# Performance work log

Hardware: AMD Instinct MI355X
Metric: run time of the kernel (lower is better)

## Reference

```python
import jax, jax.numpy as jnp
import numpy as np

B, S, I, H, O = 32, 64, 256, 256, 128


def setup_inputs() -> dict:
    key = jax.random.key(0)
    ks = jax.random.split(key, 8)
    init_k = 1.0 / np.sqrt(H)
    F = H + I
    return {
        "sentence": jax.random.normal(ks[0], (B, S, I), dtype=jnp.float32),
        "weight": jax.random.uniform(ks[1], (H, F), minval=-init_k, maxval=init_k, dtype=jnp.float32),
        "weight_lambda": jax.random.uniform(ks[2], (H, F), minval=0.0, maxval=1.0, dtype=jnp.float32),
        "weight_gamma": jax.random.uniform(ks[3], (H, F), minval=-0.001 * init_k, maxval=0.001 * init_k, dtype=jnp.float32),
        "bias": jax.random.uniform(ks[4], (H,), minval=-init_k, maxval=init_k, dtype=jnp.float32),
        "out_w": jax.random.uniform(ks[5], (O, H), minval=-init_k, maxval=init_k, dtype=jnp.float32),
        "out_b": jax.random.uniform(ks[6], (O,), minval=-init_k, maxval=init_k, dtype=jnp.float32),
    }


def reference(sentence, weight, weight_lambda, weight_gamma, bias, out_w, out_b):
    b, s, i = sentence.shape
    h_dim = weight.shape[0]
    f_dim = weight.shape[1]  # h_dim + i
    h0 = jnp.zeros((b, h_dim), dtype=sentence.dtype)
    f0 = jnp.zeros((b, h_dim, f_dim), dtype=sentence.dtype)

    def step(carry, x_t):
        h, f = carry
        total_input = jnp.concatenate([x_t, h], axis=1)          # (b, f_dim)
        total_weights = weight + f                                # (b, h, f_dim)
        pre = jnp.einsum('bf,bhf->bh', total_input, total_weights)
        norm = jnp.sqrt(jnp.sum(total_weights * total_weights, axis=2)) + 1e-16  # (b, h)
        h_new = jnp.tanh(pre / norm + bias)
        f_new = weight_lambda * (f / norm[..., None]) + \
                weight_gamma * jnp.einsum('bh,bf->bhf', h_new, total_input)
        return (h_new, f_new), None

    (h_fin, f_fin), _ = jax.lax.scan(step, (h0, f0), jnp.swapaxes(sentence, 0, 1))
    tag_space = h_fin @ out_w.T + out_b
    return tag_space, h_fin, f_fin
```

## Files before the change

kernel.cpp:

```cpp
#include <hip/hip_runtime.h>

#define Bq 32
#define Sq 64
#define Iq 256
#define Hq 256
#define Oq 128
#define Fq 512
#define WPB 8
#define NT 512

__device__ __forceinline__ float fast_tanh(float v) {
    const float e = __expf(2.0f * v);
    return 1.0f - __fdividef(2.0f, e + 1.0f);
}

__global__ __launch_bounds__(NT, 2) void stpn_main(
    const float* __restrict__ x,
    const float* __restrict__ w,
    const float* __restrict__ wl,
    const float* __restrict__ wgm,
    const float* __restrict__ bias,
    const float* __restrict__ ow,
    const float* __restrict__ ob,
    float* __restrict__ out,
    unsigned long long* __restrict__ hb)
{
    const int blk   = blockIdx.x;
    const int b     = blk & 31;
    const int chunk = blk >> 5;
    const int h0    = chunk * 32;
    const int tid   = threadIdx.x;
    const int lr    = tid & 15;
    const int r     = tid >> 4;
    const int row   = h0 + r;

    __shared__ float ti[2][Fq];

    float fw[32], fl[32], fg[32], ff[32];
    const size_t rowoff = (size_t)row * Fq;
#pragma unroll
    for (int j = 0; j < 8; ++j) {
        const int c = 4 * lr + 64 * j;
        *(float4*)&fw[4*j] = *(const float4*)(w   + rowoff + c);
        *(float4*)&fl[4*j] = *(const float4*)(wl  + rowoff + c);
        *(float4*)&fg[4*j] = *(const float4*)(wgm + rowoff + c);
    }
#pragma unroll
    for (int j = 0; j < 32; ++j) ff[j] = 0.f;

    const float brow = bias[row];
    const float* xb = x + (size_t)b * Sq * Iq;

    float nsq = 0.f;
#pragma unroll
    for (int j = 0; j < 32; ++j) nsq = fmaf(fw[j], fw[j], nsq);
#pragma unroll
    for (int m = 1; m < 16; m <<= 1) nsq += __shfl_xor(nsq, m, 16);
    float inv = __fdividef(1.0f, sqrtf(nsq) + 1e-16f);

    for (int t = 0; t < Sq; ++t) {
        const int p = t & 1;
        if (tid < Iq) {
            ti[p][tid] = xb[(size_t)t * Iq + tid];
        } else {
            const int hh = tid - Iq;
            float hv = 0.f;
            if (t > 0) {
                unsigned long long* slot =
                    hb + (size_t)((t - 1) & 1) * Bq * Hq + (size_t)b * Hq + hh;
                unsigned long long v;
                do {
                    v = __hip_atomic_load(slot, __ATOMIC_RELAXED,
                                          __HIP_MEMORY_SCOPE_AGENT);
                } while ((unsigned)(v >> 32) != (unsigned)t);
                hv = __uint_as_float((unsigned)(v & 0xffffffffu));
            }
            ti[p][Iq + hh] = hv;
        }
        __syncthreads();

        float pre = 0.f;
#pragma unroll
        for (int j = 0; j < 8; ++j) {
            const float4 tv = *(const float4*)&ti[p][4 * lr + 64 * j];
            pre = fmaf(tv.x, fw[4*j+0] + ff[4*j+0], pre);
            pre = fmaf(tv.y, fw[4*j+1] + ff[4*j+1], pre);
            pre = fmaf(tv.z, fw[4*j+2] + ff[4*j+2], pre);
            pre = fmaf(tv.w, fw[4*j+3] + ff[4*j+3], pre);
        }
#pragma unroll
        for (int m = 1; m < 16; m <<= 1) pre += __shfl_xor(pre, m, 16);
        const float hn = fast_tanh(fmaf(pre, inv, brow));

        if (lr == 0) {
            const unsigned long long pk =
                ((unsigned long long)(unsigned)(t + 1) << 32) |
                (unsigned long long)__float_as_uint(hn);
            __hip_atomic_store(
                hb + (size_t)p * Bq * Hq + (size_t)b * Hq + row, pk,
                __ATOMIC_RELAXED, __HIP_MEMORY_SCOPE_AGENT);
        }

#pragma unroll
        for (int j = 0; j < 8; ++j) {
            const float4 tv = *(const float4*)&ti[p][4 * lr + 64 * j];
            ff[4*j+0] = fmaf(fl[4*j+0], ff[4*j+0] * inv, fg[4*j+0] * (hn * tv.x));
            ff[4*j+1] = fmaf(fl[4*j+1], ff[4*j+1] * inv, fg[4*j+1] * (hn * tv.y));
            ff[4*j+2] = fmaf(fl[4*j+2], ff[4*j+2] * inv, fg[4*j+2] * (hn * tv.z));
            ff[4*j+3] = fmaf(fl[4*j+3], ff[4*j+3] * inv, fg[4*j+3] * (hn * tv.w));
        }
        if (t < Sq - 1) {
            nsq = 0.f;
#pragma unroll
            for (int j = 0; j < 32; ++j) {
                const float tw = fw[j] + ff[j];
                nsq = fmaf(tw, tw, nsq);
            }
#pragma unroll
            for (int m = 1; m < 16; m <<= 1) nsq += __shfl_xor(nsq, m, 16);
            inv = __fdividef(1.0f, sqrtf(nsq) + 1e-16f);
        }
    }

    float* fo = out + Bq * Oq + Bq * Hq + (size_t)b * Hq * Fq + rowoff;
#pragma unroll
    for (int j = 0; j < 8; ++j) {
        const int c = 4 * lr + 64 * j;
        *(float4*)(fo + c) = *(const float4*)&ff[4*j];
    }

    if (chunk == 0) {
        if (tid < Hq) {
            unsigned long long* slot =
                hb + (size_t)1 * Bq * Hq + (size_t)b * Hq + tid;
            unsigned long long v;
            do {
                v = __hip_atomic_load(slot, __ATOMIC_RELAXED,
                                      __HIP_MEMORY_SCOPE_AGENT);
            } while ((unsigned)(v >> 32) != (unsigned)Sq);
            const float hv = __uint_as_float((unsigned)(v & 0xffffffffu));
            ti[0][tid] = hv;
            out[Bq * Oq + (size_t)b * Hq + tid] = hv;
        }
        __syncthreads();
        const int o = tid >> 2;
        const int l = tid & 3;
        const float* wr = ow + (size_t)o * Hq + l * 64;
        float acc = 0.f;
#pragma unroll
        for (int k = 0; k < 16; ++k) {
            const float4 w4 = ((const float4*)wr)[k];
            const float4 h4 = *(const float4*)&ti[0][l * 64 + 4 * k];
            acc += w4.x * h4.x + w4.y * h4.y + w4.z * h4.z + w4.w * h4.w;
        }
        acc += __shfl_xor(acc, 1, 4);
        acc += __shfl_xor(acc, 2, 4);
        if (l == 0) out[(size_t)b * Oq + o] = acc + ob[o];
    }
}

extern "C" void kernel_launch(void* const* d_in, const int* in_sizes, int n_in,
                              void* d_out, int out_size, void* d_ws, size_t ws_size,
                              hipStream_t stream)
{
    const float* x    = (const float*)d_in[0];
    const float* w    = (const float*)d_in[1];
    const float* wl   = (const float*)d_in[2];
    const float* wgm  = (const float*)d_in[3];
    const float* bias = (const float*)d_in[4];
    const float* ow   = (const float*)d_in[5];
    const float* ob   = (const float*)d_in[6];
    float* out = (float*)d_out;

    hipMemsetAsync(d_ws, 0, 2 * Bq * Hq * sizeof(unsigned long long), stream);

    stpn_main<<<Bq * WPB, NT, 0, stream>>>(x, w, wl, wgm, bias, ow, ob, out,
                                           (unsigned long long*)d_ws);
}
```

Before: 182.2 us.

## Preload x into LDS, fuse norm into pre-activation pass, use precise tanh

The first 56 timesteps of each batch's input are copied into shared memory up front, so fewer global loads sit inside the serial time loop. The squared-norm reduction is fused into the pre-activation dot product and shuffle, which removes a separate pass and reduction after the f update. fast_tanh is swapped for tanhf, and the output projection indexing is changed to coalesce loads. The 56 KB of extra shared memory may cut occupancy below the 2 blocks per CU that the launch bounds request, and the grid-wide spin sync depends on all blocks being resident at once.

```diff
diff --git a/kernel.cpp b/kernel.cpp
--- a/kernel.cpp
+++ b/kernel.cpp
@@ -8,11 +8,7 @@
 #define Fq 512
 #define WPB 8
 #define NT 512
-
-__device__ __forceinline__ float fast_tanh(float v) {
-    const float e = __expf(2.0f * v);
-    return 1.0f - __fdividef(2.0f, e + 1.0f);
-}
+#define PRE_S 56
 
 __global__ __launch_bounds__(NT, 2) void stpn_main(
     const float* __restrict__ x,
@@ -35,6 +31,7 @@
     const int row   = h0 + r;
 
     __shared__ float ti[2][Fq];
+    __shared__ float xall[PRE_S * Iq];
 
     float fw[32], fl[32], fg[32], ff[32];
     const size_t rowoff = (size_t)row * Fq;
@@ -48,20 +45,20 @@
 #pragma unroll
     for (int j = 0; j < 32; ++j) ff[j] = 0.f;
 
+    {
+        const float4* xs = (const float4*)(x + (size_t)b * Sq * Iq);
+        float4* xd = (float4*)xall;
+#pragma unroll
+        for (int k = 0; k < (PRE_S * Iq / 4) / NT; ++k)
+            xd[tid + NT * k] = xs[tid + NT * k];
+    }
     const float brow = bias[row];
     const float* xb = x + (size_t)b * Sq * Iq;
-
-    float nsq = 0.f;
-#pragma unroll
-    for (int j = 0; j < 32; ++j) nsq = fmaf(fw[j], fw[j], nsq);
-#pragma unroll
-    for (int m = 1; m < 16; m <<= 1) nsq += __shfl_xor(nsq, m, 16);
-    float inv = __fdividef(1.0f, sqrtf(nsq) + 1e-16f);
 
     for (int t = 0; t < Sq; ++t) {
         const int p = t & 1;
         if (tid < Iq) {
-            ti[p][tid] = xb[(size_t)t * Iq + tid];
+            if (t >= PRE_S) ti[p][tid] = xb[(size_t)t * Iq + tid];
         } else {
             const int hh = tid - Iq;
             float hv = 0.f;
@@ -79,18 +76,35 @@
         }
         __syncthreads();
 
-        float pre = 0.f;
+        const float* xpart = (t < PRE_S) ? (xall + t * Iq) : &ti[p][0];
+        const float* hpart = &ti[p][Iq];
+
+        float pre = 0.f, nsq = 0.f;
 #pragma unroll
-        for (int j = 0; j < 8; ++j) {
-            const float4 tv = *(const float4*)&ti[p][4 * lr + 64 * j];
-            pre = fmaf(tv.x, fw[4*j+0] + ff[4*j+0], pre);
-            pre = fmaf(tv.y, fw[4*j+1] + ff[4*j+1], pre);
-            pre = fmaf(tv.z, fw[4*j+2] + ff[4*j+2], pre);
-            pre = fmaf(tv.w, fw[4*j+3] + ff[4*j+3], pre);
+        for (int j = 0; j < 4; ++j) {
+            const float4 tv = *(const float4*)&xpart[4 * lr + 64 * j];
+            float tw;
+            tw = fw[4*j+0] + ff[4*j+0]; pre = fmaf(tv.x, tw, pre); nsq = fmaf(tw, tw, nsq);
+            tw = fw[4*j+1] + ff[4*j+1]; pre = fmaf(tv.y, tw, pre); nsq = fmaf(tw, tw, nsq);
+            tw = fw[4*j+2] + ff[4*j+2]; pre = fmaf(tv.z, tw, pre); nsq = fmaf(tw, tw, nsq);
+            tw = fw[4*j+3] + ff[4*j+3]; pre = fmaf(tv.w, tw, pre); nsq = fmaf(tw, tw, nsq);
         }
 #pragma unroll
-        for (int m = 1; m < 16; m <<= 1) pre += __shfl_xor(pre, m, 16);
-        const float hn = fast_tanh(fmaf(pre, inv, brow));
+        for (int j = 4; j < 8; ++j) {
+            const float4 tv = *(const float4*)&hpart[4 * lr + 64 * (j - 4)];
+            float tw;
+            tw = fw[4*j+0] + ff[4*j+0]; pre = fmaf(tv.x, tw, pre); nsq = fmaf(tw, tw, nsq);
+            tw = fw[4*j+1] + ff[4*j+1]; pre = fmaf(tv.y, tw, pre); nsq = fmaf(tw, tw, nsq);
+            tw = fw[4*j+2] + ff[4*j+2]; pre = fmaf(tv.z, tw, pre); nsq = fmaf(tw, tw, nsq);
+            tw = fw[4*j+3] + ff[4*j+3]; pre = fmaf(tv.w, tw, pre); nsq = fmaf(tw, tw, nsq);
+        }
+#pragma unroll
+        for (int m = 1; m < 16; m <<= 1) {
+            pre += __shfl_xor(pre, m, 16);
+            nsq += __shfl_xor(nsq, m, 16);
+        }
+        const float inv = __fdividef(1.0f, sqrtf(nsq) + 1e-16f);
+        const float hn  = tanhf(fmaf(pre, inv, brow));
 
         if (lr == 0) {
             const unsigned long long pk =
@@ -102,23 +116,20 @@
         }
 
 #pragma unroll
-        for (int j = 0; j < 8; ++j) {
-            const float4 tv = *(const float4*)&ti[p][4 * lr + 64 * j];
+        for (int j = 0; j < 4; ++j) {
+            const float4 tv = *(const float4*)&xpart[4 * lr + 64 * j];
             ff[4*j+0] = fmaf(fl[4*j+0], ff[4*j+0] * inv, fg[4*j+0] * (hn * tv.x));
             ff[4*j+1] = fmaf(fl[4*j+1], ff[4*j+1] * inv, fg[4*j+1] * (hn * tv.y));
             ff[4*j+2] = fmaf(fl[4*j+2], ff[4*j+2] * inv, fg[4*j+2] * (hn * tv.z));
             ff[4*j+3] = fmaf(fl[4*j+3], ff[4*j+3] * inv, fg[4*j+3] * (hn * tv.w));
         }
-        if (t < Sq - 1) {
-            nsq = 0.f;
 #pragma unroll
-            for (int j = 0; j < 32; ++j) {
-                const float tw = fw[j] + ff[j];
-                nsq = fmaf(tw, tw, nsq);
-            }
-#pragma unroll
-            for (int m = 1; m < 16; m <<= 1) nsq += __shfl_xor(nsq, m, 16);
-            inv = __fdividef(1.0f, sqrtf(nsq) + 1e-16f);
+        for (int j = 4; j < 8; ++j) {
+            const float4 tv = *(const float4*)&hpart[4 * lr + 64 * (j - 4)];
+            ff[4*j+0] = fmaf(fl[4*j+0], ff[4*j+0] * inv, fg[4*j+0] * (hn * tv.x));
+            ff[4*j+1] = fmaf(fl[4*j+1], ff[4*j+1] * inv, fg[4*j+1] * (hn * tv.y));
+            ff[4*j+2] = fmaf(fl[4*j+2], ff[4*j+2] * inv, fg[4*j+2] * (hn * tv.z));
+            ff[4*j+3] = fmaf(fl[4*j+3], ff[4*j+3] * inv, fg[4*j+3] * (hn * tv.w));
         }
     }
 
@@ -145,12 +156,13 @@
         __syncthreads();
         const int o = tid >> 2;
         const int l = tid & 3;
-        const float* wr = ow + (size_t)o * Hq + l * 64;
+        const float* wr = ow + (size_t)o * Hq;
         float acc = 0.f;
 #pragma unroll
         for (int k = 0; k < 16; ++k) {
-            const float4 w4 = ((const float4*)wr)[k];
-            const float4 h4 = *(const float4*)&ti[0][l * 64 + 4 * k];
+            const int cc = 16 * k + 4 * l;
+            const float4 w4 = *(const float4*)(wr + cc);
+            const float4 h4 = *(const float4*)&ti[0][cc];
             acc += w4.x * h4.x + w4.y * h4.y + w4.z * h4.z + w4.w * h4.w;
         }
         acc += __shfl_xor(acc, 1, 4);
```

Measured after the change: 154.3 us. 15.3% less time.
